# Kernel tuning notes

Hardware: AMD Instinct MI355X
Metric: run time of the kernel (lower is better)

Reference implementation:

```python
import jax, jax.numpy as jnp
import numpy as np

H_IMG = 256; W_IMG = 256; C = 256
WIN = (16, 16); STRIPE = (32, 32); DF = 4; NH = 4
ASZ = (STRIPE[0] // DF, STRIPE[1] // DF)
TS = ((STRIPE[0] + ASZ[0]) // 2, (STRIPE[1] + ASZ[1]) // 2)  # stripe bias table half-size (20,20)


def _win_part(x, ws):
    # (B,H,W,c) -> (B*nW, ws0*ws1, c)
    B, H, W, c = x.shape
    x = x.reshape(B, H // ws[0], ws[0], W // ws[1], ws[1], c)
    return x.transpose(0, 1, 3, 2, 4, 5).reshape(-1, ws[0] * ws[1], c)


def _win_rev(w, ws, H, W):
    c = w.shape[-1]
    B = w.shape[0] // ((H // ws[0]) * (W // ws[1]))
    x = w.reshape(B, H // ws[0], W // ws[1], ws[0], ws[1], c)
    return x.transpose(0, 1, 3, 2, 4, 5).reshape(B, H, W, c)


def _l2n(x):
    # F.normalize(dim=-1)
    return x / jnp.maximum(jnp.linalg.norm(x, axis=-1, keepdims=True), 1e-12)


def _affine(attn, logit_scale, w1, b1, w2, table, index):
    # attn: (B_, nH, N1, N2); AffineTransform with mask=None
    N1, N2 = attn.shape[-2], attn.shape[-1]
    attn = attn * jnp.exp(jnp.minimum(logit_scale, np.log(100.0)))  # clamp max=log(1/0.01)
    bt = jax.nn.relu(table.reshape(-1, 2) @ w1 + b1) @ w2  # (T, nH)
    bias = bt[index.reshape(-1)].reshape(N1, N2, -1).transpose(2, 0, 1)  # (nH,N1,N2)
    return attn + (16.0 * jax.nn.sigmoid(bias))[None]


def _coords(start, size):
    h = np.arange(start[0], start[0] + size[0])
    w = np.arange(start[1], start[1] + size[1])
    return np.stack(np.meshgrid(h, w, indexing='ij')).reshape(2, -1)


def _idx(c1, c2, md):
    d = (c1[:, :, None] - c2[:, None, :]).transpose(1, 2, 0).astype(np.int64)
    return (d[..., 0] + md[0] - 1) * (2 * md[1] - 1) + (d[..., 1] + md[1] - 1)


def _table(ts):
    h = np.arange(-(ts[0] - 1), ts[0], dtype=np.float32) / (ts[0] - 1)
    w = np.arange(-(ts[1] - 1), ts[1], dtype=np.float32) / (ts[1] - 1)
    t = np.stack(np.meshgrid(h, w, indexing='ij'), axis=-1)[None] * 8.0
    return (np.sign(t) * np.log2(np.abs(t) + 1.0) / np.log2(8.0)).astype(np.float32)


def setup_inputs():
    ks = iter(jax.random.split(jax.random.key(0), 32))
    def nrm(shape, s=0.02):
        return jax.random.normal(next(ks), shape, dtype=jnp.float32) * s
    inp = {}
    inp['x'] = jax.random.normal(next(ks), (1, H_IMG * W_IMG, C), dtype=jnp.float32)
    inp['qkv_w'] = nrm((C, 3 * C)); inp['qkv_b'] = nrm((3 * C,))
    inp['anchor_w'] = nrm((C, C // 2)); inp['anchor_b'] = nrm((C // 2,))
    for tag in ['w', 's1', 's2']:
        inp['ls_' + tag] = jnp.full((NH, 1, 1), np.log(10.0), dtype=jnp.float32)
        inp['cpb_w1_' + tag] = nrm((2, 512), 0.1)
        inp['cpb_b1_' + tag] = nrm((512,), 0.1)
        inp['cpb_w2_' + tag] = nrm((512, NH), 0.1)
    inp['proj_w'] = nrm((C, C)); inp['proj_b'] = nrm((C,))
    inp['table_w'] = jnp.asarray(_table(WIN))
    inp['table_s'] = jnp.asarray(_table(TS))
    cw = _coords((0, 0), WIN)
    inp['index_w'] = jnp.asarray(_idx(cw, cw, WIN), dtype=jnp.int32)
    cs = _coords((0, 0), STRIPE)
    st = ((STRIPE[0] - ASZ[0]) // 2, (STRIPE[1] - ASZ[1]) // 2)
    ca = _coords(st, ASZ)
    inp['index_a2w'] = jnp.asarray(_idx(ca, cs, TS), dtype=jnp.int32)
    inp['index_w2a'] = jnp.asarray(_idx(cs, ca, TS), dtype=jnp.int32)
    return inp


def reference(x, qkv_w, qkv_b, anchor_w, anchor_b,
              ls_w, cpb_w1_w, cpb_b1_w, cpb_w2_w,
              ls_s1, cpb_w1_s1, cpb_b1_s1, cpb_w2_s1,
              ls_s2, cpb_w1_s2, cpb_b1_s2, cpb_w2_s2,
              proj_w, proj_b, table_w, table_s,
              index_w, index_a2w, index_w2a):
    B, L, c = x.shape
    qkv = x @ qkv_w + qkv_b               # (B, L, 3C)
    half = 3 * c // 2
    hd = half // 3 // NH                  # head_dim per branch
    # ---- window attention on first half of qkv channels ----
    qw = _win_part(qkv[..., :half].reshape(B, H_IMG, W_IMG, half), WIN)  # (B_, N, 3*C/2)
    B_, N, _ = qw.shape
    q, k, v = qw.reshape(B_, N, 3, NH, hd).transpose(2, 0, 3, 1, 4)
    attn = jnp.einsum('bhnd,bhmd->bhnm', _l2n(q), _l2n(k))
    attn = jax.nn.softmax(_affine(attn, ls_w, cpb_w1_w, cpb_b1_w, cpb_w2_w, table_w, index_w), axis=-1)
    xw = jnp.einsum('bhnm,bhmd->bhnd', attn, v).transpose(0, 2, 1, 3).reshape(B_, N, NH * hd)
    xw = _win_rev(xw, WIN, H_IMG, W_IMG).reshape(B, L, c // 2)
    # ---- anchor projection: AvgPool2d(DF) + Linear(C -> C/2) ----
    xi = x.reshape(B, H_IMG, W_IMG, c)
    pooled = xi.reshape(B, H_IMG // DF, DF, W_IMG // DF, DF, c).mean(axis=(2, 4))
    anchor = pooled @ anchor_w + anchor_b  # (B, H/DF, W/DF, C/2)
    # ---- anchor stripe attention on second half ----
    qs = _win_part(qkv[..., half:].reshape(B, H_IMG, W_IMG, half), STRIPE)  # (Bs, N1, 3*C/2)
    Bs, N1, _ = qs.shape
    anc = _win_part(anchor, ASZ)           # (Bs, N2, C/2)
    N2 = anc.shape[1]
    q, k, v = qs.reshape(Bs, N1, 3, NH, hd).transpose(2, 0, 3, 1, 4)
    anc = anc.reshape(Bs, N2, NH, hd).transpose(0, 2, 1, 3)
    a1 = jnp.einsum('bhnd,bhmd->bhnm', _l2n(anc), _l2n(k))   # (Bs,NH,N2,N1)
    a1 = jax.nn.softmax(_affine(a1, ls_s1, cpb_w1_s1, cpb_b1_s1, cpb_w2_s1, table_s, index_a2w), axis=-1)
    xm = jnp.einsum('bhnm,bhmd->bhnd', a1, v)                # (Bs,NH,N2,hd)
    a2 = jnp.einsum('bhnd,bhmd->bhnm', _l2n(q), _l2n(anc))   # (Bs,NH,N1,N2)
    a2 = jax.nn.softmax(_affine(a2, ls_s2, cpb_w1_s2, cpb_b1_s2, cpb_w2_s2, table_s, index_w2a), axis=-1)
    xs = jnp.einsum('bhnm,bhmd->bhnd', a2, xm).transpose(0, 2, 1, 3).reshape(Bs, N1, NH * hd)
    xs = _win_rev(xs, STRIPE, H_IMG, W_IMG).reshape(B, L, c // 2)
    # ---- merge + output projection ----
    return jnp.concatenate([xw, xs], axis=-1) @ proj_w + proj_b
```

## Files before the change

### kernel.cpp

```cpp
#include <hip/hip_runtime.h>
#include <cstdint>
#include <cstddef>

typedef unsigned short u16;
typedef __attribute__((ext_vector_type(8))) short short8;
typedef __attribute__((ext_vector_type(4))) float floatx4;
typedef __attribute__((ext_vector_type(2))) float floatx2;
typedef __attribute__((ext_vector_type(4))) unsigned int uintx4;
typedef __attribute__((ext_vector_type(2))) unsigned int uintx2;
typedef __attribute__((ext_vector_type(2))) __bf16 bf16x2;

#define LOG2E 1.44269504f

__device__ __forceinline__ float bf2f(u16 u){
  union { unsigned int i; float f; } v; v.i = ((unsigned int)u) << 16; return v.f;
}
__device__ __forceinline__ u16 f2bf(float f){
  union { __bf16 b; u16 u; } v; v.b = (__bf16)f; return v.u;
}
__device__ __forceinline__ unsigned int pk2(float a, float b){
  union { bf16x2 h; unsigned int u; } v;
  v.h = __builtin_convertvector((floatx2){a, b}, bf16x2);
  return v.u;
}
__device__ __forceinline__ void gload16(const void* g, void* l){
  __builtin_amdgcn_global_load_lds((const __attribute__((address_space(1))) unsigned int*)g,
                                   (__attribute__((address_space(3))) unsigned int*)l, 16, 0, 0);
}
__device__ __forceinline__ uintx4 ld8f_bf(const float* g){
  floatx4 u0 = *(const floatx4*)g;
  floatx4 u1 = *(const floatx4*)(g + 4);
  uintx4 w;
  w.x = pk2(u0.x, u0.y); w.y = pk2(u0.z, u0.w);
  w.z = pk2(u1.x, u1.y); w.w = pk2(u1.z, u1.w);
  return w;
}
__device__ __forceinline__ float redq(float v){
  v += __shfl_xor(v, 16); v += __shfl_xor(v, 32);
  return v;
}

__global__ void transpose_w(const float* __restrict__ qkv_w, const float* __restrict__ anchor_w,
                            const float* __restrict__ proj_w,
                            u16* __restrict__ qkvt, u16* __restrict__ anct, u16* __restrict__ projt){
  int id = blockIdx.x*256 + threadIdx.x;
  if (id < 196608){ int k = id / 768, n = id % 768; qkvt[n*256 + k] = f2bf(qkv_w[id]); }
  else if (id < 229376){ int r = id - 196608; int k = r / 128, n = r % 128; anct[n*256 + k] = f2bf(anchor_w[r]); }
  else { int r = id - 229376; int k = r >> 8, n = r & 255; projt[n*256 + k] = f2bf(proj_w[r]); }
}

__global__ void cpb_mlp(const float* __restrict__ tw, const float* __restrict__ ts,
                        const float* __restrict__ w1w, const float* __restrict__ b1w, const float* __restrict__ w2w,
                        const float* __restrict__ w1s1, const float* __restrict__ b1s1, const float* __restrict__ w2s1,
                        const float* __restrict__ w1s2, const float* __restrict__ b1s2, const float* __restrict__ w2s2,
                        float* __restrict__ btw, float* __restrict__ bts1, float* __restrict__ bts2){
  int tag = blockIdx.y;
  const float *tab, *w1, *b1, *w2; float* bt; int T;
  if (tag == 0){ tab = tw; w1 = w1w;  b1 = b1w;  w2 = w2w;  bt = btw;  T = 961; }
  else if (tag == 1){ tab = ts; w1 = w1s1; b1 = b1s1; w2 = w2s1; bt = bts1; T = 1521; }
  else { tab = ts; w1 = w1s2; b1 = b1s2; w2 = w2s2; bt = bts2; T = 1521; }
  __shared__ float sw1[2][512];
  __shared__ float sb1[512];
  __shared__ float sw2[512][4];
  for (int j = threadIdx.x; j < 512; j += 256){
    sw1[0][j] = w1[j]; sw1[1][j] = w1[512 + j]; sb1[j] = b1[j];
    for (int h = 0; h < 4; ++h) sw2[j][h] = w2[j*4 + h];
  }
  __syncthreads();
  int idx = blockIdx.x*256 + threadIdx.x;
  int r = idx >> 2, hh = idx & 3;
  if (r < T){
    float t0 = tab[2*r], t1 = tab[2*r + 1];
    float acc = 0.f;
    for (int j = 0; j < 512; ++j){
      float hj = fmaxf(fmaf(t0, sw1[0][j], fmaf(t1, sw1[1][j], sb1[j])), 0.f);
      acc = fmaf(hj, sw2[j][hh], acc);
    }
    bt[r*4 + hh] = acc;
  }
}

__global__ void bias_gather(const float* __restrict__ btw, const float* __restrict__ bts1,
                            const float* __restrict__ bts2,
                            const int* __restrict__ idxw, const int* __restrict__ idxa2w,
                            const int* __restrict__ idxw2a,
                            const float* __restrict__ lsw, const float* __restrict__ ls1,
                            const float* __restrict__ ls2,
                            float* __restrict__ bw, float* __restrict__ bs1, float* __restrict__ bs2){
  int id = blockIdx.x*256 + threadIdx.x;
  int which = id >> 18;
  int rem = id & 262143;
  int h = rem >> 16, e = rem & 65535;
  const float* bt; const int* ix; float* dst; const float* ls;
  if (which == 0){ bt = btw;  ix = idxw;   dst = bw;  ls = lsw; }
  else if (which == 1){ bt = bts1; ix = idxa2w; dst = bs1; ls = ls1; }
  else { bt = bts2; ix = idxw2a; dst = bs2; ls = ls2; }
  float v = bt[ix[e]*4 + h];
  float scale = exp2f(fminf(ls[h], 4.6051702f) * LOG2E);
  float off = fminf(scale + 16.f, 80.f);
  float sig = 16.f / (1.f + exp2f(-v * LOG2E));
  dst[h*65536 + e] = (sig - off) * LOG2E;
}

__global__ void avgpool(const float* __restrict__ x, float* __restrict__ pooled){
  int a = blockIdx.x, c = threadIdx.x;
  int ay = a >> 6, ax = a & 63;
  float acc = 0.f;
#pragma unroll
  for (int dy = 0; dy < 4; ++dy)
#pragma unroll
    for (int dx = 0; dx < 4; ++dx)
      acc += x[(size_t)((ay*4 + dy)*256 + ax*4 + dx)*256 + c];
  pooled[(size_t)a*256 + c] = acc * 0.0625f;
}

__launch_bounds__(256, 2)
__global__ void gemm_qkv(const float* __restrict__ A, const u16* __restrict__ Bt,
                         const float* __restrict__ bias, u16* __restrict__ C,
                         u16* __restrict__ VTg, int N, int K){
  __shared__ __align__(16) u16 lsA[4096];
  __shared__ __align__(16) u16 lsB[4096];
  const int tid = threadIdx.x, lane = tid & 63, wv = tid >> 6;
  const int lane15 = lane & 15, quad = lane >> 4;
  const int wr = wv >> 1, wc = wv & 1;
  const int m0 = blockIdx.x * 128;
  const int y = blockIdx.y;
  const bool vmode = (y == 2);
  const u16* Btb = Bt + (size_t)y*128*K;
  const float* bb = bias + y*128;
  char* lsBb = (char*)lsB;
  const int brow = wv*16 + (lane >> 2);
  const u16* bsrc = Btb + (size_t)brow*K + (lane & 3)*8;
  const int arow = tid & 127, aq = tid >> 7;
  const float* asrc = A + (size_t)(m0 + arow)*K;
  const int aslot0 = aq*1024 + ((arow + aq*2) & 127)*8;
  const int aslot1 = (aq+2)*1024 + ((arow + (aq+2)*2) & 127)*8;
  floatx4 acc[4][4] = {};
  for (int k0 = 0; k0 < K; k0 += 32){
    gload16(bsrc + k0,                 lsBb + wv*1024);
    gload16(bsrc + (size_t)64*K + k0,  lsBb + 4096 + wv*1024);
    uintx4 ra0 = ld8f_bf(asrc + k0 + aq*8);
    uintx4 ra1 = ld8f_bf(asrc + k0 + (aq+2)*8);
    *(uintx4*)(lsA + aslot0) = ra0;
    *(uintx4*)(lsA + aslot1) = ra1;
    __syncthreads();
    short8 a[4], b[4];
#pragma unroll
    for (int i = 0; i < 4; ++i){
      int r = wr*64 + i*16 + lane15;
      a[i] = *(const short8*)(lsA + quad*1024 + ((r + quad*2) & 127)*8);
    }
#pragma unroll
    for (int j = 0; j < 4; ++j)
      b[j] = *(const short8*)(lsBb + (wc*64 + j*16 + lane15)*64 + quad*16);
    if (!vmode){
#pragma unroll
      for (int i = 0; i < 4; ++i)
#pragma unroll
        for (int j = 0; j < 4; ++j)
          acc[i][j] = __builtin_amdgcn_mfma_f32_16x16x32_bf16(b[j], a[i], acc[i][j], 0, 0, 0);
    } else {
#pragma unroll
      for (int i = 0; i < 4; ++i)
#pragma unroll
        for (int j = 0; j < 4; ++j)
          acc[i][j] = __builtin_amdgcn_mfma_f32_16x16x32_bf16(a[i], b[j], acc[i][j], 0, 0, 0);
    }
    __syncthreads();
  }
  if (vmode){
#pragma unroll
    for (int j = 0; j < 4; ++j){
      int col = wc*64 + j*16 + lane15;
      float bz = bb[col];
#pragma unroll
      for (int i = 0; i < 4; ++i){
        int rowb = m0 + wr*64 + i*16 + quad*4;
        uintx2 w;
        w.x = pk2(acc[i][j][0] + bz, acc[i][j][1] + bz);
        w.y = pk2(acc[i][j][2] + bz, acc[i][j][3] + bz);
        *(uintx2*)(VTg + (size_t)col*32768 + rowb) = w;
      }
    }
  } else {
#pragma unroll
    for (int j = 0; j < 4; ++j){
      floatx4 bz = *(const floatx4*)(bb + wc*64 + j*16 + quad*4);
#pragma unroll
      for (int i = 0; i < 4; ++i) acc[i][j] += bz;
    }
#pragma unroll
    for (int i = 0; i < 4; ++i){
#pragma unroll
      for (int jp = 0; jp < 2; ++jp){
        floatx4 s2 = acc[i][jp*2]*acc[i][jp*2] + acc[i][jp*2+1]*acc[i][jp*2+1];
        float ss = (s2.x + s2.y) + (s2.z + s2.w);
        ss = redq(ss);
        float inv = 1.f / fmaxf(sqrtf(ss), 1e-12f);
        acc[i][jp*2]   *= inv;
        acc[i][jp*2+1] *= inv;
      }
    }
#pragma unroll
    for (int i = 0; i < 4; ++i){
      int row = m0 + wr*64 + i*16 + lane15;
#pragma unroll
      for (int j = 0; j < 4; ++j){
        int colb = y*128 + wc*64 + j*16 + quad*4;
        uintx2 w;
        w.x = pk2(acc[i][j][0], acc[i][j][1]);
        w.y = pk2(acc[i][j][2], acc[i][j][3]);
        *(uintx2*)(C + (size_t)row*N + colb) = w;
      }
    }
  }
}

__launch_bounds__(256, 2)
__global__ void gemm_proj_inplace(float* __restrict__ AC, const u16* __restrict__ Bt,
                                  const float* __restrict__ bias){
  __shared__ __align__(16) u16 lsA[4096];
  __shared__ __align__(16) u16 lsB[8192];
  const int tid = threadIdx.x, lane = tid & 63, wv = tid >> 6;
  const int lane15 = lane & 15, quad = lane >> 4;
  const int wr = wv >> 1, wc = wv & 1;
  const int m0 = blockIdx.x * 128;
  char* lsBb = (char*)lsB;
  const int brow = wv*16 + (lane >> 2);
  const u16* bsrc = Bt + (size_t)brow*256 + (lane & 3)*8;
  const int arow = tid & 127, aq = tid >> 7;
  const float* asrc = AC + (size_t)(m0 + arow)*256;
  const int aslot0 = aq*1024 + ((arow + aq*2) & 127)*8;
  const int aslot1 = (aq+2)*1024 + ((arow + (aq+2)*2) & 127)*8;
  floatx4 acc[4][8] = {};
  for (int k0 = 0; k0 < 256; k0 += 32){
    gload16(bsrc + k0,                lsBb +         wv*1024);
    gload16(bsrc + 64*256 + k0,       lsBb + 4096  + wv*1024);
    gload16(bsrc + 128*256 + k0,      lsBb + 8192  + wv*1024);
    gload16(bsrc + 192*256 + k0,      lsBb + 12288 + wv*1024);
    uintx4 ra0 = ld8f_bf(asrc + k0 + aq*8);
    uintx4 ra1 = ld8f_bf(asrc + k0 + (aq+2)*8);
    *(uintx4*)(lsA + aslot0) = ra0;
    *(uintx4*)(lsA + aslot1) = ra1;
    __syncthreads();
    short8 a[4], b[8];
#pragma unroll
    for (int i = 0; i < 4; ++i){
      int r = wr*64 + i*16 + lane15;
      a[i] = *(const short8*)(lsA + quad*1024 + ((r + quad*2) & 127)*8);
    }
#pragma unroll
    for (int j = 0; j < 8; ++j)
      b[j] = *(const short8*)(lsBb + (wc*128 + j*16 + lane15)*64 + quad*16);
#pragma unroll
    for (int i = 0; i < 4; ++i)
#pragma unroll
      for (int j = 0; j < 8; ++j)
        acc[i][j] = __builtin_amdgcn_mfma_f32_16x16x32_bf16(b[j], a[i], acc[i][j], 0, 0, 0);
    __syncthreads();
  }
#pragma unroll
  for (int i = 0; i < 4; ++i){
    int row = m0 + wr*64 + i*16 + lane15;
#pragma unroll
    for (int j = 0; j < 8; ++j){
      int colb = wc*128 + j*16 + quad*4;
      floatx4 bz = *(const floatx4*)(bias + colb);
      floatx4 o = acc[i][j] + bz;
      *(floatx4*)(AC + (size_t)row*256 + colb) = o;
    }
  }
}

__launch_bounds__(256, 3)
__global__ void win_attn(const u16* __restrict__ qkvh, const u16* __restrict__ vt,
                         const float* __restrict__ lsw,
                         const float* __restrict__ biasw, float* __restrict__ outm, int r0){
  __shared__ __align__(16) u16 sm[16384];
  const int tid = threadIdx.x, lane = tid & 63, wv = tid >> 6;
  const int lane15 = lane & 15, quad = lane >> 4;
  const int h = blockIdx.y;
  const int wyl = blockIdx.x >> 4, wx = blockIdx.x & 15;
  u16* Ks = sm;
  u16* Qs = sm + 8192;
  {
    int tok = wv*64 + lane;
    int row = (wyl*16 + (tok >> 4))*256 + wx*16 + (tok & 15);
    const char* src = (const char*)(qkvh + (size_t)row*256) + h*64;
    char* qd = (char*)Qs + wv*1024;
    char* kd = (char*)Ks + wv*1024;
#pragma unroll
    for (int kq = 0; kq < 4; ++kq){
      gload16(src + kq*16,        qd + kq*4096);
      gload16(src + 256 + kq*16,  kd + kq*4096);
    }
  }
  __syncthreads();
  short8 qf[4];
#pragma unroll
  for (int j = 0; j < 4; ++j)
    qf[j] = *(const short8*)(Qs + quad*2048 + (wv*64 + j*16 + lane15)*8);
  __syncthreads();

  float scale = exp2f(fminf(lsw[h], 4.6051702f) * LOG2E) * LOG2E;
  const float* bptr = biasw + ((size_t)h << 16);
  const u16* vbase = vt + (size_t)(h*32)*32768;
  u16* Pw = Qs + wv*2048;
  const floatx4 zf4 = {0.f, 0.f, 0.f, 0.f};
  floatx4 accO[2][4] = {};
  float lsum[4] = {};

  for (int kc = 0; kc < 8; ++kc){
    int key0 = kc*32 + quad*8;
    int krow = (wyl*16 + (key0 >> 4))*256 + wx*16 + (key0 & 15);
    short8 vtf[2];
#pragma unroll
    for (int m = 0; m < 2; ++m)
      vtf[m] = *(const short8*)(vbase + (size_t)(m*16 + lane15)*32768 + krow);
    floatx4 bia[2][4];
#pragma unroll
    for (int i = 0; i < 2; ++i)
#pragma unroll
      for (int j = 0; j < 4; ++j)
        bia[i][j] = *(const floatx4*)(bptr + (size_t)(wv*64 + j*16 + lane15)*256 + kc*32 + i*16 + quad*4);
    short8 kf[2];
#pragma unroll
    for (int i = 0; i < 2; ++i)
      kf[i] = *(const short8*)(Ks + quad*2048 + (kc*32 + i*16 + lane15)*8);
#pragma unroll
    for (int i = 0; i < 2; ++i)
#pragma unroll
      for (int j = 0; j < 4; ++j){
        floatx4 sv = __builtin_amdgcn_mfma_f32_16x16x32_bf16(kf[i], qf[j], zf4, 0, 0, 0);
        float p0 = exp2f(fmaf(sv[0], scale, bia[i][j][0]));
        float p1 = exp2f(fmaf(sv[1], scale, bia[i][j][1]));
        float p2 = exp2f(fmaf(sv[2], scale, bia[i][j][2]));
        float p3 = exp2f(fmaf(sv[3], scale, bia[i][j][3]));
        lsum[j] += (p0 + p1) + (p2 + p3);
        uintx2 w; w.x = pk2(p0, p1); w.y = pk2(p2, p3);
        *(uintx2*)(Pw + (i*2 + (quad>>1))*512 + (j*16 + lane15)*8 + (quad&1)*4) = w;
      }
    asm volatile("s_waitcnt lgkmcnt(0)" ::: "memory");
    short8 ptf[4];
#pragma unroll
    for (int j = 0; j < 4; ++j)
      ptf[j] = *(const short8*)(Pw + quad*512 + (j*16 + lane15)*8);
#pragma unroll
    for (int m = 0; m < 2; ++m)
#pragma unroll
      for (int j = 0; j < 4; ++j)
        accO[m][j] = __builtin_amdgcn_mfma_f32_16x16x32_bf16(vtf[m], ptf[j], accO[m][j], 0, 0, 0);
  }
  float linv[4];
#pragma unroll
  for (int j = 0; j < 4; ++j) linv[j] = 1.f / redq(lsum[j]);
#pragma unroll
  for (int m = 0; m < 2; ++m)
#pragma unroll
    for (int j = 0; j < 4; ++j){
      int tok = wv*64 + j*16 + lane15;
      int py = r0 + wyl*16 + (tok >> 4), px = wx*16 + (tok & 15);
      floatx4 o = accO[m][j] * linv[j];
      *(floatx4*)(outm + (size_t)(py*256 + px)*256 + h*32 + m*16 + quad*4) = o;
    }
}

__launch_bounds__(256, 3)
__global__ void stripe_xm(const u16* __restrict__ qkvh, const u16* __restrict__ vt,
                          const u16* __restrict__ anchor,
                          const float* __restrict__ ls1, const float* __restrict__ bias1,
                          float* __restrict__ gl1, u16* __restrict__ gO, int r0){
  __shared__ __align__(16) u16 sm[18432];
  const int tid = threadIdx.x, lane = tid & 63, wv = tid >> 6;
  const int lane15 = lane & 15, quad = lane >> 4;
  const int s = blockIdx.x, h = blockIdx.y, kb = blockIdx.z;
  const int syl = s >> 3, sx = s & 7;
  u16* ANC = sm; u16* P1T = sm + 10240;
  if (wv == 0){
    int ay = (r0 >> 2) + syl*8 + (lane >> 3), ax = sx*8 + (lane & 7);
    const char* asrc = (const char*)(anchor + (size_t)(ay*64 + ax)*128) + h*64;
#pragma unroll
    for (int kq = 0; kq < 4; ++kq)
      gload16(asrc + kq*16, (char*)ANC + kq*1024);
  }
  auto stageK = [&](int kc, int buf){
    int kkb = kb*512 + kc*128;
    char* KC = (char*)(sm + 2048 + buf*4096);
#pragma unroll
    for (int hf = 0; hf < 2; ++hf){
      int tok = kkb + hf*64 + lane;
      int row = (syl*32 + (tok >> 5))*256 + sx*32 + (tok & 31);
      gload16((const char*)(qkvh + (size_t)row*256) + 256 + h*64 + wv*16,
              KC + wv*2048 + hf*1024);
    }
  };
  stageK(0, 0);
  __syncthreads();
  short8 ancf = *(const short8*)(ANC + quad*512 + (wv*16 + lane15)*8);
  float scale1 = exp2f(fminf(ls1[h], 4.6051702f) * LOG2E) * LOG2E;
  const float* b1p = bias1 + ((size_t)h << 16) + (size_t)(wv*16 + lane15)*1024;
  const u16* vbase = vt + (size_t)(h*32)*32768;
  const floatx4 zf4 = {0.f, 0.f, 0.f, 0.f};
  floatx4 accO1[2] = {};
  float l1 = 0.f;
  for (int kc = 0; kc < 4; ++kc){
    if (kc < 3) stageK(kc + 1, (kc + 1) & 1);
    int kkb = kb*512 + kc*128;
    const u16* KC = sm + 2048 + (kc & 1)*4096;
    short8 vfrag[4][2];
#pragma unroll
    for (int ks = 0; ks < 4; ++ks){
      int key0 = kkb + (ks*4 + quad)*8;
      int krow = (syl*32 + (key0 >> 5))*256 + sx*32 + (key0 & 31);
#pragma unroll
      for (int m = 0; m < 2; ++m)
        vfrag[ks][m] = *(const short8*)(vbase + (size_t)(m*16 + lane15)*32768 + krow);
    }
    floatx4 bia[8];
#pragma unroll
    for (int i = 0; i < 8; ++i)
      bia[i] = *(const floatx4*)(b1p + kkb + i*16 + quad*4);
#pragma unroll
    for (int i = 0; i < 8; ++i){
      short8 kf = *(const short8*)(KC + quad*1024 + (i*16 + lane15)*8);
      floatx4 sv = __builtin_amdgcn_mfma_f32_16x16x32_bf16(kf, ancf, zf4, 0, 0, 0);
      float p0 = exp2f(fmaf(sv[0], scale1, bia[i][0]));
      float p1 = exp2f(fmaf(sv[1], scale1, bia[i][1]));
      float p2 = exp2f(fmaf(sv[2], scale1, bia[i][2]));
      float p3 = exp2f(fmaf(sv[3], scale1, bia[i][3]));
      l1 += (p0 + p1) + (p2 + p3);
      uintx2 w; w.x = pk2(p0, p1); w.y = pk2(p2, p3);
      *(uintx2*)(P1T + (i*2 + (quad>>1))*512 + (wv*16 + lane15)*8 + (quad&1)*4) = w;
    }
    asm volatile("s_waitcnt lgkmcnt(0)" ::: "memory");
#pragma unroll
    for (int ks = 0; ks < 4; ++ks){
      short8 ptf = *(const short8*)(P1T + (ks*4 + quad)*512 + (wv*16 + lane15)*8);
#pragma unroll
      for (int m = 0; m < 2; ++m)
        accO1[m] = __builtin_amdgcn_mfma_f32_16x16x32_bf16(vfrag[ks][m], ptf, accO1[m], 0, 0, 0);
    }
    __syncthreads();
  }
  l1 = redq(l1);
  int ent = (s*4 + h)*2 + kb;
  if (quad == 0) gl1[ent*64 + wv*16 + lane15] = l1;
#pragma unroll
  for (int m = 0; m < 2; ++m){
    uintx2 w; w.x = pk2(accO1[m][0], accO1[m][1]); w.y = pk2(accO1[m][2], accO1[m][3]);
    *(uintx2*)(gO + (size_t)ent*2048 + (wv*16 + lane15)*32 + m*16 + quad*4) = w;
  }
}

__launch_bounds__(256, 3)
__global__ void stripe_xs(const u16* __restrict__ qkvh, const u16* __restrict__ anchor,
                          const float* __restrict__ ls2, const float* __restrict__ bias2,
                          const float* __restrict__ gl1, const u16* __restrict__ gO,
                          float* __restrict__ outm, int r0){
  __shared__ __align__(16) u16 sm[20480];
  const int tid = threadIdx.x, lane = tid & 63, wv = tid >> 6;
  const int lane15 = lane & 15, quad = lane >> 4;
  const int s = blockIdx.x >> 2, qc = blockIdx.x & 3, h = blockIdx.y;
  const int syl = s >> 3, sx = s & 7;
  u16* ANC = sm;
  u16* XMT = sm + 2048;
  u16* QW  = sm + 4096 + wv*2048;
  u16* P2T = sm + 12288 + wv*2048;
  if (wv == 0){
    int ay = (r0 >> 2) + syl*8 + (lane >> 3), ax = sx*8 + (lane & 7);
    const char* asrc = (const char*)(anchor + (size_t)(ay*64 + ax)*128) + h*64;
#pragma unroll
    for (int kq = 0; kq < 4; ++kq)
      gload16(asrc + kq*16, (char*)ANC + kq*1024);
  }
  {
    int a = tid >> 2, db = (tid & 3)*8;
    int e0 = (s*4 + h)*2;
    float inv = 1.f / (gl1[e0*64 + a] + gl1[(e0 + 1)*64 + a]);
    uintx4 u0 = *(const uintx4*)(gO + (size_t)e0*2048 + a*32 + db);
    uintx4 u1 = *(const uintx4*)(gO + (size_t)(e0 + 1)*2048 + a*32 + db);
    unsigned int w0[4] = {u0.x, u0.y, u0.z, u0.w};
    unsigned int w1[4] = {u1.x, u1.y, u1.z, u1.w};
#pragma unroll
    for (int c = 0; c < 4; ++c){
      float a0 = bf2f((u16)(w0[c] & 0xffffu)) + bf2f((u16)(w1[c] & 0xffffu));
      float a1 = bf2f((u16)(w0[c] >> 16))     + bf2f((u16)(w1[c] >> 16));
      XMT[(a >> 3)*256 + (db + c*2)*8     + (a & 7)] = f2bf(a0 * inv);
      XMT[(a >> 3)*256 + (db + c*2 + 1)*8 + (a & 7)] = f2bf(a1 * inv);
    }
  }
  int tq = qc*256 + wv*64;
  {
    int tok = tq + lane;
    int row = (syl*32 + (tok >> 5))*256 + sx*32 + (tok & 31);
    const char* src = (const char*)(qkvh + (size_t)row*256) + h*64;
#pragma unroll
    for (int kq = 0; kq < 4; ++kq)
      gload16(src + kq*16, (char*)QW + kq*1024);
  }
  __syncthreads();
  short8 qf2[4];
#pragma unroll
  for (int j = 0; j < 4; ++j)
    qf2[j] = *(const short8*)(QW + quad*512 + (j*16 + lane15)*8);
  float scale2 = exp2f(fminf(ls2[h], 4.6051702f) * LOG2E) * LOG2E;
  const float* b2p = bias2 + ((size_t)h << 16);
  const floatx4 zf4 = {0.f, 0.f, 0.f, 0.f};
  floatx4 accO2[2][4] = {};
  float l2[4] = {};
#pragma unroll
  for (int c = 0; c < 2; ++c){
    floatx4 bia[2][4];
#pragma unroll
    for (int i = 0; i < 2; ++i)
#pragma unroll
      for (int j = 0; j < 4; ++j)
        bia[i][j] = *(const floatx4*)(b2p + (size_t)(tq + j*16 + lane15)*64 + c*32 + i*16 + quad*4);
    short8 af[2];
#pragma unroll
    for (int i = 0; i < 2; ++i)
      af[i] = *(const short8*)(ANC + quad*512 + (c*32 + i*16 + lane15)*8);
#pragma unroll
    for (int i = 0; i < 2; ++i)
#pragma unroll
      for (int j = 0; j < 4; ++j){
        floatx4 sv = __builtin_amdgcn_mfma_f32_16x16x32_bf16(af[i], qf2[j], zf4, 0, 0, 0);
        float p0 = exp2f(fmaf(sv[0], scale2, bia[i][j][0]));
        float p1 = exp2f(fmaf(sv[1], scale2, bia[i][j][1]));
        float p2 = exp2f(fmaf(sv[2], scale2, bia[i][j][2]));
        float p3 = exp2f(fmaf(sv[3], scale2, bia[i][j][3]));
        l2[j] += (p0 + p1) + (p2 + p3);
        uintx2 w; w.x = pk2(p0, p1); w.y = pk2(p2, p3);
        *(uintx2*)(P2T + (i*2 + (quad>>1))*512 + (j*16 + lane15)*8 + (quad&1)*4) = w;
      }
    asm volatile("s_waitcnt lgkmcnt(0)" ::: "memory");
    short8 ptf[4], xmf[2];
#pragma unroll
    for (int j = 0; j < 4; ++j)
      ptf[j] = *(const short8*)(P2T + quad*512 + (j*16 + lane15)*8);
#pragma unroll
    for (int m = 0; m < 2; ++m)
      xmf[m] = *(const short8*)(XMT + (c*4 + quad)*256 + (m*16 + lane15)*8);
#pragma unroll
    for (int m = 0; m < 2; ++m)
#pragma unroll
      for (int j = 0; j < 4; ++j)
        accO2[m][j] = __builtin_amdgcn_mfma_f32_16x16x32_bf16(xmf[m], ptf[j], accO2[m][j], 0, 0, 0);
  }
  float linv[4];
#pragma unroll
  for (int j = 0; j < 4; ++j) linv[j] = 1.f / redq(l2[j]);
#pragma unroll
  for (int m = 0; m < 2; ++m)
#pragma unroll
    for (int j = 0; j < 4; ++j){
      int tok = tq + j*16 + lane15;
      int py = r0 + syl*32 + (tok >> 5), px = sx*32 + (tok & 31);
      floatx4 o = accO2[m][j] * linv[j];
      *(floatx4*)(outm + (size_t)(py*256 + px)*256 + 128 + h*32 + m*16 + quad*4) = o;
    }
}

extern "C" void kernel_launch(void* const* d_in, const int* in_sizes, int n_in,
                              void* d_out, int out_size, void* d_ws, size_t ws_size,
                              hipStream_t stream) {
  (void)in_sizes; (void)n_in; (void)out_size; (void)ws_size;
  const float* x        = (const float*)d_in[0];
  const float* qkv_w    = (const float*)d_in[1];
  const float* qkv_b    = (const float*)d_in[2];
  const float* anchor_w = (const float*)d_in[3];
  const float* anchor_b = (const float*)d_in[4];
  const float* ls_w     = (const float*)d_in[5];
  const float* w1_w     = (const float*)d_in[6];
  const float* b1_w     = (const float*)d_in[7];
  const float* w2_w     = (const float*)d_in[8];
  const float* ls_s1    = (const float*)d_in[9];
  const float* w1_s1    = (const float*)d_in[10];
  const float* b1_s1    = (const float*)d_in[11];
  const float* w2_s1    = (const float*)d_in[12];
  const float* ls_s2    = (const float*)d_in[13];
  const float* w1_s2    = (const float*)d_in[14];
  const float* b1_s2    = (const float*)d_in[15];
  const float* w2_s2    = (const float*)d_in[16];
  const float* proj_w   = (const float*)d_in[17];
  const float* proj_b   = (const float*)d_in[18];
  const float* table_w  = (const float*)d_in[19];
  const float* table_s  = (const float*)d_in[20];
  const int* index_w   = (const int*)d_in[21];
  const int* index_a2w = (const int*)d_in[22];
  const int* index_w2a = (const int*)d_in[23];

  char* ws = (char*)d_ws;
  u16*   qkvh   = (u16*)(ws + 0);
  float* pooled = (float*)(ws + 0);
  u16*   vt     = (u16*)(ws + 16777216);
  u16*   anch   = (u16*)(ws + 25165824);
  u16*   qkvt   = (u16*)(ws + 26214400);
  u16*   anct   = (u16*)(ws + 26607616);
  u16*   projt  = (u16*)(ws + 26673152);
  float* btw    = (float*)(ws + 26804224);
  float* bts1   = (float*)(ws + 26820608);
  float* bts2   = (float*)(ws + 26845184);
  float* biasw  = (float*)(ws + 26869760);
  float* bias1  = (float*)(ws + 27918336);
  float* bias2  = (float*)(ws + 28966912);
  float* gl1    = (float*)(ws + 30015488);
  u16*   gO     = (u16*)(ws + 30081024);

  float* merged = (float*)d_out;

  transpose_w<<<1152, 256, 0, stream>>>(qkv_w, anchor_w, proj_w, qkvt, anct, projt);
  cpb_mlp<<<dim3(24, 3), 256, 0, stream>>>(table_w, table_s,
                                           w1_w, b1_w, w2_w,
                                           w1_s1, b1_s1, w2_s1,
                                           w1_s2, b1_s2, w2_s2,
                                           btw, bts1, bts2);
  bias_gather<<<3072, 256, 0, stream>>>(btw, bts1, bts2, index_w, index_a2w, index_w2a,
                                        ls_w, ls_s1, ls_s2, biasw, bias1, bias2);
  avgpool<<<4096, 256, 0, stream>>>(x, pooled);
  gemm_qkv<<<dim3(32, 1), 256, 0, stream>>>(pooled, anct, anchor_b, anch, vt, 128, 256);

  for (int half = 0; half < 2; ++half){
    const float* xh = x + (size_t)half*32768*256;
    int r0 = half*128;
    gemm_qkv<<<dim3(256, 3), 256, 0, stream>>>(xh, qkvt, qkv_b, qkvh, vt, 256, 256);
    win_attn<<<dim3(128, 4), 256, 0, stream>>>(qkvh, vt, ls_w, biasw, merged, r0);
    gemm_qkv<<<dim3(256, 3), 256, 0, stream>>>(xh, qkvt + 384*256, qkv_b + 384, qkvh, vt, 256, 256);
    stripe_xm<<<dim3(32, 4, 2), 256, 0, stream>>>(qkvh, vt, anch, ls_s1, bias1, gl1, gO, r0);
    stripe_xs<<<dim3(128, 4), 256, 0, stream>>>(qkvh, anch, ls_s2, bias2, gl1, gO, merged, r0);
  }

  gemm_proj_inplace<<<dim3(512), 256, 0, stream>>>(merged, projt, proj_b);
}
```

Before: 423.4 us.

## Keep V row-major in qkv buffer, transpose in LDS, pre-swizzle bias tables

The QKV GEMM no longer writes V transposed into a separate global buffer with column strides. It now writes all three projections row-major into one 384-wide qkvh buffer. The window and stripe attention kernels load V rows and transpose them into shared memory themselves. bias_gather also writes the relative-position bias tables in the exact fragment order the MFMA loops read, so each bias load is contiguous and coalesced. This trades uncoalesced global stores and strided V fragment loads for extra LDS capacity and scalar 16-bit LDS transpose writes, which may hit bank conflicts and may lower occupancy.

Result: faster. 396.6 us (-6.3%).

```diff
diff --git a/kernel.cpp b/kernel.cpp
--- a/kernel.cpp
+++ b/kernel.cpp
@@ -99,7 +99,19 @@
   float scale = exp2f(fminf(ls[h], 4.6051702f) * LOG2E);
   float off = fminf(scale + 16.f, 80.f);
   float sig = 16.f / (1.f + exp2f(-v * LOG2E));
-  dst[h*65536 + e] = (sig - off) * LOG2E;
+  float out = (sig - off) * LOG2E;
+  int idx;
+  if (which == 0){
+    int q = e >> 8, k = e & 255;
+    idx = ((((h*8 + (k>>5))*2 + ((k>>4)&1))*4 + ((k>>2)&3)) << 10) + (q << 2) + (k & 3);
+  } else if (which == 1){
+    int a = e >> 10, k = e & 1023;
+    idx = (((h*64 + (k>>4))*4 + ((k>>2)&3)) << 8) + (a << 2) + (k & 3);
+  } else {
+    int q = e >> 6, k = e & 63;
+    idx = (((h*4 + (k>>4))*4 + ((k>>2)&3)) << 12) + (q << 2) + (k & 3);
+  }
+  dst[idx] = out;
 }
 
 __global__ void avgpool(const float* __restrict__ x, float* __restrict__ pooled){
@@ -117,7 +129,7 @@
 __launch_bounds__(256, 2)
 __global__ void gemm_qkv(const float* __restrict__ A, const u16* __restrict__ Bt,
                          const float* __restrict__ bias, u16* __restrict__ C,
-                         u16* __restrict__ VTg, int N, int K){
+                         int N, int K){
   __shared__ __align__(16) u16 lsA[4096];
   __shared__ __align__(16) u16 lsB[4096];
   const int tid = threadIdx.x, lane = tid & 63, wv = tid >> 6;
@@ -125,7 +137,6 @@
   const int wr = wv >> 1, wc = wv & 1;
   const int m0 = blockIdx.x * 128;
   const int y = blockIdx.y;
-  const bool vmode = (y == 2);
   const u16* Btb = Bt + (size_t)y*128*K;
   const float* bb = bias + y*128;
   char* lsBb = (char*)lsB;
@@ -153,42 +164,20 @@
 #pragma unroll
     for (int j = 0; j < 4; ++j)
       b[j] = *(const short8*)(lsBb + (wc*64 + j*16 + lane15)*64 + quad*16);
-    if (!vmode){
-#pragma unroll
-      for (int i = 0; i < 4; ++i)
-#pragma unroll
-        for (int j = 0; j < 4; ++j)
-          acc[i][j] = __builtin_amdgcn_mfma_f32_16x16x32_bf16(b[j], a[i], acc[i][j], 0, 0, 0);
-    } else {
-#pragma unroll
-      for (int i = 0; i < 4; ++i)
-#pragma unroll
-        for (int j = 0; j < 4; ++j)
-          acc[i][j] = __builtin_amdgcn_mfma_f32_16x16x32_bf16(a[i], b[j], acc[i][j], 0, 0, 0);
-    }
+#pragma unroll
+    for (int i = 0; i < 4; ++i)
+#pragma unroll
+      for (int j = 0; j < 4; ++j)
+        acc[i][j] = __builtin_amdgcn_mfma_f32_16x16x32_bf16(b[j], a[i], acc[i][j], 0, 0, 0);
     __syncthreads();
   }
-  if (vmode){
-#pragma unroll
-    for (int j = 0; j < 4; ++j){
-      int col = wc*64 + j*16 + lane15;
-      float bz = bb[col];
-#pragma unroll
-      for (int i = 0; i < 4; ++i){
-        int rowb = m0 + wr*64 + i*16 + quad*4;
-        uintx2 w;
-        w.x = pk2(acc[i][j][0] + bz, acc[i][j][1] + bz);
-        w.y = pk2(acc[i][j][2] + bz, acc[i][j][3] + bz);
-        *(uintx2*)(VTg + (size_t)col*32768 + rowb) = w;
-      }
-    }
-  } else {
-#pragma unroll
-    for (int j = 0; j < 4; ++j){
-      floatx4 bz = *(const floatx4*)(bb + wc*64 + j*16 + quad*4);
-#pragma unroll
-      for (int i = 0; i < 4; ++i) acc[i][j] += bz;
-    }
+#pragma unroll
+  for (int j = 0; j < 4; ++j){
+    floatx4 bz = *(const floatx4*)(bb + wc*64 + j*16 + quad*4);
+#pragma unroll
+    for (int i = 0; i < 4; ++i) acc[i][j] += bz;
+  }
+  if (y < 2){
 #pragma unroll
     for (int i = 0; i < 4; ++i){
 #pragma unroll
@@ -201,17 +190,17 @@
         acc[i][jp*2+1] *= inv;
       }
     }
-#pragma unroll
-    for (int i = 0; i < 4; ++i){
-      int row = m0 + wr*64 + i*16 + lane15;
-#pragma unroll
-      for (int j = 0; j < 4; ++j){
-        int colb = y*128 + wc*64 + j*16 + quad*4;
-        uintx2 w;
-        w.x = pk2(acc[i][j][0], acc[i][j][1]);
-        w.y = pk2(acc[i][j][2], acc[i][j][3]);
-        *(uintx2*)(C + (size_t)row*N + colb) = w;
-      }
+  }
+#pragma unroll
+  for (int i = 0; i < 4; ++i){
+    int row = m0 + wr*64 + i*16 + lane15;
+#pragma unroll
+    for (int j = 0; j < 4; ++j){
+      int colb = y*128 + wc*64 + j*16 + quad*4;
+      uintx2 w;
+      w.x = pk2(acc[i][j][0], acc[i][j][1]);
+      w.y = pk2(acc[i][j][2], acc[i][j][3]);
+      *(uintx2*)(C + (size_t)row*N + colb) = w;
     }
   }
 }
@@ -273,26 +262,35 @@
 }
 
 __launch_bounds__(256, 3)
-__global__ void win_attn(const u16* __restrict__ qkvh, const u16* __restrict__ vt,
-                         const float* __restrict__ lsw,
+__global__ void win_attn(const u16* __restrict__ qkvh, const float* __restrict__ lsw,
                          const float* __restrict__ biasw, float* __restrict__ outm, int r0){
-  __shared__ __align__(16) u16 sm[16384];
+  __shared__ __align__(16) u16 sm[24576];
   const int tid = threadIdx.x, lane = tid & 63, wv = tid >> 6;
   const int lane15 = lane & 15, quad = lane >> 4;
   const int h = blockIdx.y;
   const int wyl = blockIdx.x >> 4, wx = blockIdx.x & 15;
   u16* Ks = sm;
   u16* Qs = sm + 8192;
+  u16* VT = sm + 16384;
   {
     int tok = wv*64 + lane;
     int row = (wyl*16 + (tok >> 4))*256 + wx*16 + (tok & 15);
-    const char* src = (const char*)(qkvh + (size_t)row*256) + h*64;
-    char* qd = (char*)Qs + wv*1024;
-    char* kd = (char*)Ks + wv*1024;
+    const char* src = (const char*)qkvh + (size_t)row*768 + h*64;
 #pragma unroll
     for (int kq = 0; kq < 4; ++kq){
-      gload16(src + kq*16,        qd + kq*4096);
-      gload16(src + 256 + kq*16,  kd + kq*4096);
+      gload16(src + kq*16,        (char*)Qs + wv*1024 + kq*4096);
+      gload16(src + 256 + kq*16,  (char*)Ks + wv*1024 + kq*4096);
+    }
+    int vrow = (wyl*16 + (tid >> 4))*256 + wx*16 + (tid & 15);
+    const uintx4* vp = (const uintx4*)((const char*)qkvh + (size_t)vrow*768 + 512 + h*64);
+    uintx4 v0 = vp[0], v1 = vp[1], v2 = vp[2], v3 = vp[3];
+    unsigned int w[16] = {v0.x,v0.y,v0.z,v0.w, v1.x,v1.y,v1.z,v1.w,
+                          v2.x,v2.y,v2.z,v2.w, v3.x,v3.y,v3.z,v3.w};
+    u16* vd = VT + (tid >> 3)*256 + (tid & 7);
+#pragma unroll
+    for (int c = 0; c < 16; ++c){
+      vd[(c*2)*8]   = (u16)(w[c] & 0xffffu);
+      vd[(c*2+1)*8] = (u16)(w[c] >> 16);
     }
   }
   __syncthreads();
@@ -303,26 +301,19 @@
   __syncthreads();
 
   float scale = exp2f(fminf(lsw[h], 4.6051702f) * LOG2E) * LOG2E;
-  const float* bptr = biasw + ((size_t)h << 16);
-  const u16* vbase = vt + (size_t)(h*32)*32768;
   u16* Pw = Qs + wv*2048;
   const floatx4 zf4 = {0.f, 0.f, 0.f, 0.f};
   floatx4 accO[2][4] = {};
   float lsum[4] = {};
 
   for (int kc = 0; kc < 8; ++kc){
-    int key0 = kc*32 + quad*8;
-    int krow = (wyl*16 + (key0 >> 4))*256 + wx*16 + (key0 & 15);
-    short8 vtf[2];
-#pragma unroll
-    for (int m = 0; m < 2; ++m)
-      vtf[m] = *(const short8*)(vbase + (size_t)(m*16 + lane15)*32768 + krow);
     floatx4 bia[2][4];
 #pragma unroll
     for (int i = 0; i < 2; ++i)
 #pragma unroll
       for (int j = 0; j < 4; ++j)
-        bia[i][j] = *(const floatx4*)(bptr + (size_t)(wv*64 + j*16 + lane15)*256 + kc*32 + i*16 + quad*4);
+        bia[i][j] = *(const floatx4*)(biasw + ((((h*8 + kc)*2 + i)*4 + quad) << 10)
+                                            + ((wv*64 + j*16 + lane15) << 2));
     short8 kf[2];
 #pragma unroll
     for (int i = 0; i < 2; ++i)
@@ -341,10 +332,13 @@
         *(uintx2*)(Pw + (i*2 + (quad>>1))*512 + (j*16 + lane15)*8 + (quad&1)*4) = w;
       }
     asm volatile("s_waitcnt lgkmcnt(0)" ::: "memory");
-    short8 ptf[4];
+    short8 ptf[4], vtf[2];
 #pragma unroll
     for (int j = 0; j < 4; ++j)
       ptf[j] = *(const short8*)(Pw + quad*512 + (j*16 + lane15)*8);
+#pragma unroll
+    for (int m = 0; m < 2; ++m)
+      vtf[m] = *(const short8*)(VT + (kc*4 + quad)*256 + (m*16 + lane15)*8);
 #pragma unroll
     for (int m = 0; m < 2; ++m)
 #pragma unroll
@@ -366,60 +360,63 @@
 }
 
 __launch_bounds__(256, 3)
-__global__ void stripe_xm(const u16* __restrict__ qkvh, const u16* __restrict__ vt,
-                          const u16* __restrict__ anchor,
+__global__ void stripe_xm(const u16* __restrict__ qkvh, const u16* __restrict__ anchor,
                           const float* __restrict__ ls1, const float* __restrict__ bias1,
                           float* __restrict__ gl1, u16* __restrict__ gO, int r0){
-  __shared__ __align__(16) u16 sm[18432];
+  __shared__ __align__(16) u16 sm[22528];
   const int tid = threadIdx.x, lane = tid & 63, wv = tid >> 6;
   const int lane15 = lane & 15, quad = lane >> 4;
   const int s = blockIdx.x, h = blockIdx.y, kb = blockIdx.z;
   const int syl = s >> 3, sx = s & 7;
-  u16* ANC = sm; u16* P1T = sm + 10240;
+  u16* ANC = sm; u16* VT = sm + 10240; u16* P1T = sm + 14336;
   if (wv == 0){
     int ay = (r0 >> 2) + syl*8 + (lane >> 3), ax = sx*8 + (lane & 7);
-    const char* asrc = (const char*)(anchor + (size_t)(ay*64 + ax)*128) + h*64;
+    const char* asrc = (const char*)anchor + (size_t)(ay*64 + ax)*256 + h*64;
 #pragma unroll
     for (int kq = 0; kq < 4; ++kq)
       gload16(asrc + kq*16, (char*)ANC + kq*1024);
   }
-  auto stageK = [&](int kc, int buf){
+  auto stageK = [&](int kc){
     int kkb = kb*512 + kc*128;
-    char* KC = (char*)(sm + 2048 + buf*4096);
+    char* KC = (char*)sm + 4096 + (kc & 1)*8192;
 #pragma unroll
     for (int hf = 0; hf < 2; ++hf){
       int tok = kkb + hf*64 + lane;
       int row = (syl*32 + (tok >> 5))*256 + sx*32 + (tok & 31);
-      gload16((const char*)(qkvh + (size_t)row*256) + 256 + h*64 + wv*16,
+      gload16((const char*)qkvh + (size_t)row*768 + 256 + h*64 + wv*16,
               KC + wv*2048 + hf*1024);
     }
   };
-  stageK(0, 0);
-  __syncthreads();
-  short8 ancf = *(const short8*)(ANC + quad*512 + (wv*16 + lane15)*8);
+  stageK(0);
   float scale1 = exp2f(fminf(ls1[h], 4.6051702f) * LOG2E) * LOG2E;
-  const float* b1p = bias1 + ((size_t)h << 16) + (size_t)(wv*16 + lane15)*1024;
-  const u16* vbase = vt + (size_t)(h*32)*32768;
   const floatx4 zf4 = {0.f, 0.f, 0.f, 0.f};
   floatx4 accO1[2] = {};
   float l1 = 0.f;
   for (int kc = 0; kc < 4; ++kc){
-    if (kc < 3) stageK(kc + 1, (kc + 1) & 1);
     int kkb = kb*512 + kc*128;
+    {
+      int tok_l = tid >> 1, dh = tid & 1;
+      int tok = kkb + tok_l;
+      int row = (syl*32 + (tok >> 5))*256 + sx*32 + (tok & 31);
+      const uintx4* vp = (const uintx4*)((const char*)qkvh + (size_t)row*768 + 512 + h*64 + dh*32);
+      uintx4 v0 = vp[0], v1 = vp[1];
+      unsigned int w[8] = {v0.x,v0.y,v0.z,v0.w, v1.x,v1.y,v1.z,v1.w};
+      u16* vd = VT + (tok_l >> 3)*256 + dh*128 + (tok_l & 7);
+#pragma unroll
+      for (int c = 0; c < 8; ++c){
+        vd[(c*2)*8]   = (u16)(w[c] & 0xffffu);
+        vd[(c*2+1)*8] = (u16)(w[c] >> 16);
+      }
+    }
+    __syncthreads();
+    if (kc < 3) stageK(kc + 1);
     const u16* KC = sm + 2048 + (kc & 1)*4096;
-    short8 vfrag[4][2];
-#pragma unroll
-    for (int ks = 0; ks < 4; ++ks){
-      int key0 = kkb + (ks*4 + quad)*8;
-      int krow = (syl*32 + (key0 >> 5))*256 + sx*32 + (key0 & 31);
-#pragma unroll
-      for (int m = 0; m < 2; ++m)
-        vfrag[ks][m] = *(const short8*)(vbase + (size_t)(m*16 + lane15)*32768 + krow);
-    }
+    short8 ancf = *(const short8*)(ANC + quad*512 + (wv*16 + lane15)*8);
     floatx4 bia[8];
 #pragma unroll
     for (int i = 0; i < 8; ++i)
-      bia[i] = *(const floatx4*)(b1p + kkb + i*16 + quad*4);
+      bia[i] = *(const floatx4*)(bias1 + (((h*64 + kb*32 + kc*8 + i)*4 + quad) << 8)
+                                       + ((wv*16 + lane15) << 2));
 #pragma unroll
     for (int i = 0; i < 8; ++i){
       short8 kf = *(const short8*)(KC + quad*1024 + (i*16 + lane15)*8);
@@ -437,8 +434,10 @@
     for (int ks = 0; ks < 4; ++ks){
       short8 ptf = *(const short8*)(P1T + (ks*4 + quad)*512 + (wv*16 + lane15)*8);
 #pragma unroll
-      for (int m = 0; m < 2; ++m)
-        accO1[m] = __builtin_amdgcn_mfma_f32_16x16x32_bf16(vfrag[ks][m], ptf, accO1[m], 0, 0, 0);
+      for (int m = 0; m < 2; ++m){
+        short8 vtf = *(const short8*)(VT + (ks*4 + quad)*256 + (m*16 + lane15)*8);
+        accO1[m] = __builtin_amdgcn_mfma_f32_16x16x32_bf16(vtf, ptf, accO1[m], 0, 0, 0);
+      }
     }
     __syncthreads();
   }
@@ -468,7 +467,7 @@
   u16* P2T = sm + 12288 + wv*2048;
   if (wv == 0){
     int ay = (r0 >> 2) + syl*8 + (lane >> 3), ax = sx*8 + (lane & 7);
-    const char* asrc = (const char*)(anchor + (size_t)(ay*64 + ax)*128) + h*64;
+    const char* asrc = (const char*)anchor + (size_t)(ay*64 + ax)*256 + h*64;
 #pragma unroll
     for (int kq = 0; kq < 4; ++kq)
       gload16(asrc + kq*16, (char*)ANC + kq*1024);
@@ -493,7 +492,7 @@
   {
     int tok = tq + lane;
     int row = (syl*32 + (tok >> 5))*256 + sx*32 + (tok & 31);
-    const char* src = (const char*)(qkvh + (size_t)row*256) + h*64;
+    const char* src = (const char*)qkvh + (size_t)row*768 + h*64;
 #pragma unroll
     for (int kq = 0; kq < 4; ++kq)
       gload16(src + kq*16, (char*)QW + kq*1024);
@@ -504,7 +503,6 @@
   for (int j = 0; j < 4; ++j)
     qf2[j] = *(const short8*)(QW + quad*512 + (j*16 + lane15)*8);
   float scale2 = exp2f(fminf(ls2[h], 4.6051702f) * LOG2E) * LOG2E;
-  const float* b2p = bias2 + ((size_t)h << 16);
   const floatx4 zf4 = {0.f, 0.f, 0.f, 0.f};
   floatx4 accO2[2][4] = {};
   float l2[4] = {};
@@ -515,7 +513,8 @@
     for (int i = 0; i < 2; ++i)
 #pragma unroll
       for (int j = 0; j < 4; ++j)
-        bia[i][j] = *(const floatx4*)(b2p + (size_t)(tq + j*16 + lane15)*64 + c*32 + i*16 + quad*4);
+        bia[i][j] = *(const floatx4*)(bias2 + ((((h*4 + c*2 + i)*4 + quad) << 12)
+                                             + ((tq + j*16 + lane15) << 2)));
     short8 af[2];
 #pragma unroll
     for (int i = 0; i < 2; ++i)
@@ -593,7 +592,6 @@
   char* ws = (char*)d_ws;
   u16*   qkvh   = (u16*)(ws + 0);
   float* pooled = (float*)(ws + 0);
-  u16*   vt     = (u16*)(ws + 16777216);
   u16*   anch   = (u16*)(ws + 25165824);
   u16*   qkvt   = (u16*)(ws + 26214400);
   u16*   anct   = (u16*)(ws + 26607616);
@@ -618,15 +616,15 @@
   bias_gather<<<3072, 256, 0, stream>>>(btw, bts1, bts2, index_w, index_a2w, index_w2a,
                                         ls_w, ls_s1, ls_s2, biasw, bias1, bias2);
   avgpool<<<4096, 256, 0, stream>>>(x, pooled);
-  gemm_qkv<<<dim3(32, 1), 256, 0, stream>>>(pooled, anct, anchor_b, anch, vt, 128, 256);
+  gemm_qkv<<<dim3(32, 1), 256, 0, stream>>>(pooled, anct, anchor_b, anch, 128, 256);
 
   for (int half = 0; half < 2; ++half){
     const float* xh = x + (size_t)half*32768*256;
     int r0 = half*128;
-    gemm_qkv<<<dim3(256, 3), 256, 0, stream>>>(xh, qkvt, qkv_b, qkvh, vt, 256, 256);
-    win_attn<<<dim3(128, 4), 256, 0, stream>>>(qkvh, vt, ls_w, biasw, merged, r0);
-    gemm_qkv<<<dim3(256, 3), 256, 0, stream>>>(xh, qkvt + 384*256, qkv_b + 384, qkvh, vt, 256, 256);
-    stripe_xm<<<dim3(32, 4, 2), 256, 0, stream>>>(qkvh, vt, anch, ls_s1, bias1, gl1, gO, r0);
+    gemm_qkv<<<dim3(256, 3), 256, 0, stream>>>(xh, qkvt, qkv_b, qkvh, 384, 256);
+    win_attn<<<dim3(128, 4), 256, 0, stream>>>(qkvh, ls_w, biasw, merged, r0);
+    gemm_qkv<<<dim3(256, 3), 256, 0, stream>>>(xh, qkvt + 384*256, qkv_b + 384, qkvh, 384, 256);
+    stripe_xm<<<dim3(32, 4, 2), 256, 0, stream>>>(qkvh, anch, ls_s1, bias1, gl1, gO, r0);
     stripe_xs<<<dim3(128, 4), 256, 0, stream>>>(qkvh, anch, ls_s2, bias2, gl1, gO, merged, r0);
   }
 
```
